# Optimization experiments

Hardware: AMD Instinct MI355X
Metric: run time of the kernel (lower is better)

Reference implementation:

```python
import jax, jax.numpy as jnp
import numpy as np
import math

HID = 128      # hidden_dim == d_inner (expand=1)
NSTATE = 8     # d_state
K = 4          # scan directions
RANK = math.ceil(HID / 16)  # dt_rank = 8
B, H, W = 4, 64, 64


def _ln(x, g, b, eps=1e-5):
    m = jnp.mean(x, -1, keepdims=True)
    v = jnp.mean((x - m) ** 2, -1, keepdims=True)
    return (x - m) * jax.lax.rsqrt(v + eps) * g + b


def _ss2d(x, in_w, conv_w, conv_b, xproj_w, dt_w, dt_b, A_logs, Ds, ln_g, ln_b, out_w):
    # x: [B,H,W,C] -> VMamba SS2D with d_inner=C, 4-direction selective scan
    Bn, Hh, Ww, C = x.shape
    D, L = C, Hh * Ww
    N = A_logs.shape[-1]
    R = dt_w.shape[-1]
    xz = x @ in_w.T                      # [B,H,W,2D]
    xc, z = jnp.split(xz, 2, axis=-1)
    xc = xc.transpose(0, 3, 1, 2)        # [B,D,H,W]
    xc = jax.lax.conv_general_dilated(xc, conv_w, (1, 1), 'SAME', feature_group_count=D)
    xc = jax.nn.silu(xc + conv_b[None, :, None, None])
    x_hw = xc.reshape(Bn, D, L)
    x_wh = xc.transpose(0, 1, 3, 2).reshape(Bn, D, L)
    xs = jnp.stack([x_hw, x_wh, x_hw[..., ::-1], x_wh[..., ::-1]], 1)  # [B,K,D,L]
    x_dbl = jnp.einsum('bkdl,kcd->bkcl', xs, xproj_w)
    dts, Bs, Cs = x_dbl[:, :, :R], x_dbl[:, :, R:R + N], x_dbl[:, :, R + N:]
    dt = jax.nn.softplus(jnp.einsum('bkrl,kdr->bkdl', dts, dt_w) + dt_b[None, :, :, None])
    A = -jnp.exp(A_logs.reshape(K, D, N))  # [K,D,N]

    def step(h, inp):
        x_t, dt_t, B_t, C_t = inp          # [B,K,D],[B,K,D],[B,K,N],[B,K,N]
        h = h * jnp.exp(dt_t[..., None] * A) + dt_t[..., None] * B_t[:, :, None, :] * x_t[..., None]
        return h, jnp.einsum('bkdn,bkn->bkd', h, C_t)

    h0 = jnp.zeros((Bn, K, D, N), x.dtype)
    _, ys = jax.lax.scan(step, h0, (xs.transpose(3, 0, 1, 2), dt.transpose(3, 0, 1, 2),
                                    Bs.transpose(3, 0, 1, 2), Cs.transpose(3, 0, 1, 2)))
    out_y = ys.transpose(1, 2, 3, 0) + Ds.reshape(K, D)[None, :, :, None] * xs  # [B,K,D,L]
    wh_y = out_y[:, 3, :, ::-1].reshape(Bn, D, Ww, Hh).transpose(0, 1, 3, 2).reshape(Bn, D, L)
    invwh_y = out_y[:, 1].reshape(Bn, D, Ww, Hh).transpose(0, 1, 3, 2).reshape(Bn, D, L)
    y = out_y[:, 0] + out_y[:, 2, :, ::-1] + wh_y + invwh_y
    y = _ln(y.transpose(0, 2, 1).reshape(Bn, Hh, Ww, D), ln_g, ln_b)
    return (y * jax.nn.silu(z)) @ out_w.T


def _enhance(x, g, b, w, bias):
    return jax.nn.gelu(_ln(x, g, b) @ w.T + bias, approximate=False)


def setup_inputs() -> dict:
    key = jax.random.key(0)
    ks = jax.random.split(key, 12)
    f = lambda k, s, sc=0.02: jax.random.normal(k, s, jnp.float32) * sc
    return dict(
        sar_feat=jax.random.normal(ks[0], (B, H, W, HID), jnp.float32),
        opt_feat=jax.random.normal(ks[1], (B, H, W, HID), jnp.float32),
        ss_in_w=f(ks[2], (2, 2 * HID, HID)),
        ss_conv_w=f(ks[3], (2, HID, 1, 3, 3), 0.1),
        ss_conv_b=f(ks[4], (2, HID)),
        ss_xproj_w=f(ks[5], (2, K, RANK + 2 * NSTATE, HID)),
        ss_dt_w=f(ks[6], (2, K, HID, RANK), 0.1),
        ss_dt_b=f(ks[7], (2, K, HID), 0.1),
        ss_Alogs=jnp.tile(jnp.log(jnp.arange(1, NSTATE + 1, dtype=jnp.float32)), (2, K * HID, 1)),
        ss_Ds=jnp.ones((2, K * HID), jnp.float32),
        ss_ln_g=jnp.ones((2, HID), jnp.float32),
        ss_ln_b=jnp.zeros((2, HID), jnp.float32),
        ss_out_w=f(ks[8], (2, HID, HID)),
        enh_ln_g=jnp.ones((2, HID), jnp.float32),
        enh_ln_b=jnp.zeros((2, HID), jnp.float32),
        enh_w=f(ks[9], (2, HID, HID)),
        enh_b=jnp.zeros((2, HID), jnp.float32),
    )


def reference(sar_feat, opt_feat, ss_in_w, ss_conv_w, ss_conv_b, ss_xproj_w, ss_dt_w,
              ss_dt_b, ss_Alogs, ss_Ds, ss_ln_g, ss_ln_b, ss_out_w,
              enh_ln_g, enh_ln_b, enh_w, enh_b):
    # cat([opt,sar],-1)[...,:C] == opt ; cat([sar,opt],-1)[...,:C] == sar (faithful identity slice)
    # index 0 = cross_ss2d_s2o (input opt), index 1 = cross_ss2d_o2s (input sar)
    xin = jnp.stack([opt_feat, sar_feat])
    guided = jax.vmap(_ss2d)(xin, ss_in_w, ss_conv_w, ss_conv_b, ss_xproj_w, ss_dt_w,
                             ss_dt_b, ss_Alogs, ss_Ds, ss_ln_g, ss_ln_b, ss_out_w)
    # enhance params: index 0 = enhance_sar (on sar_guided=guided[1]), index 1 = enhance_opt (on opt_guided=guided[0])
    enh_in = jnp.stack([guided[1], guided[0]])
    enhanced = jax.vmap(_enhance)(enh_in, enh_ln_g, enh_ln_b, enh_w, enh_b)
    return (sar_feat + enhanced[0], opt_feat + enhanced[1])
```

## Files before the change

kernel.cpp:

```cpp
#include <hip/hip_runtime.h>
#include <hip/hip_bf16.h>
#include <math.h>

#define DEV __device__ __forceinline__

static constexpr int LL = 4096;
static constexpr int DD = 128;
static constexpr int SEG = 128;
static constexpr float LOG2E = 1.4426950408889634f;
static constexpr float LN2 = 0.6931471805599453f;

DEV float silu_(float x) { return x / (1.f + __expf(-x)); }
DEV float erf_(float x) {
  const float ax = fabsf(x);
  const float t = 1.f / fmaf(0.3275911f, ax, 1.f);
  float p = fmaf(1.061405429f, t, -1.453152027f);
  p = fmaf(p, t, 1.421413741f);
  p = fmaf(p, t, -0.284496736f);
  p = fmaf(p, t, 0.254829592f);
  p = p * t;
  const float r = 1.f - p * __expf(-ax * ax);
  return x < 0.f ? -r : r;
}
DEV float gelu_(float x) { return 0.5f * x * (1.f + erf_(x * 0.7071067811865475f)); }
DEV float sp_(float x) {
  const float t = __builtin_amdgcn_exp2f(-fabsf(x) * LOG2E);
  return fmaxf(x, 0.f) + LN2 * __builtin_amdgcn_logf(1.f + t);
}

template <int CTRL>
DEV float dpp_add_(float x) {
  int y = __builtin_amdgcn_update_dpp(0, __float_as_int(x), CTRL, 0xF, 0xF, true);
  return x + __int_as_float(y);
}

DEV void seg_base_step(int k, int s, int& base, int& step) {
  if (k == 0)      { base = s * 64;        step = 1;   }
  else if (k == 1) { base = s;             step = 64;  }
  else if (k == 2) { base = 4095 - s * 64; step = -1;  }
  else             { base = 4095 - s;      step = -64; }
}

__global__ __launch_bounds__(256) void k_inproj(
    const float* __restrict__ sar, const float* __restrict__ opt,
    const float* __restrict__ in_w, float* __restrict__ xz) {
  const int lt = blockIdx.x, ct = blockIdx.y, mb = blockIdx.z;
  const int m = mb >> 2;
  const float* __restrict__ x = (m == 0 ? opt : sar) + (size_t)(mb & 3) * (LL * DD);
  const float* __restrict__ W = in_w + (size_t)m * 256 * DD;
  __shared__ float sA[64][68];
  __shared__ float sW[64][68];
  const int tid = threadIdx.x;
  const int tc = tid & 15, tl = tid >> 4;
  float acc[4][4] = {};
  for (int db = 0; db < 2; ++db) {
    __syncthreads();
    for (int idx = tid; idx < 64 * 16; idx += 256) {
      const int r = idx >> 4, d4 = (idx & 15) << 2;
      *(float4*)&sA[r][d4] = *(const float4*)&x[(size_t)(lt * 64 + r) * DD + db * 64 + d4];
      *(float4*)&sW[r][d4] = *(const float4*)&W[(size_t)(ct * 64 + r) * DD + db * 64 + d4];
    }
    __syncthreads();
#pragma unroll 4
    for (int d = 0; d < 64; d += 4) {
      float4 a[4], w[4];
#pragma unroll
      for (int q = 0; q < 4; ++q) a[q] = *(const float4*)&sA[tl * 4 + q][d];
#pragma unroll
      for (int j = 0; j < 4; ++j) w[j] = *(const float4*)&sW[tc + 16 * j][d];
#pragma unroll
      for (int j = 0; j < 4; ++j)
#pragma unroll
        for (int q = 0; q < 4; ++q)
          acc[j][q] += a[q].x * w[j].x + a[q].y * w[j].y + a[q].z * w[j].z + a[q].w * w[j].w;
    }
  }
  float* __restrict__ dst = xz + ((size_t)mb * 256 + ct * 64) * LL + lt * 64;
#pragma unroll
  for (int j = 0; j < 4; ++j) {
    float4 v = make_float4(acc[j][0], acc[j][1], acc[j][2], acc[j][3]);
    *(float4*)&dst[(size_t)(tc + 16 * j) * LL + tl * 4] = v;
  }
}

__global__ __launch_bounds__(256) void k_conv(
    const float* __restrict__ xz, const float* __restrict__ conv_w,
    const float* __restrict__ conv_b, float* __restrict__ xc) {
  const int ht = blockIdx.x, dg = blockIdx.y, mb = blockIdx.z;
  const int m = mb >> 2;
  __shared__ float sIn[8][18][66];
  __shared__ float sOut[1024][8];
  const float* __restrict__ src = xz + ((size_t)mb * 256 + dg * 8) * LL;
  const int tid = threadIdx.x;
  for (int idx = tid; idx < 8 * 18 * 66; idx += 256) {
    const int dd = idx / (18 * 66);
    const int rem = idx - dd * (18 * 66);
    const int hh = rem / 66, ww = rem - hh * 66;
    const int h = ht * 16 + hh - 1, w = ww - 1;
    float v = 0.f;
    if (h >= 0 && h < 64 && w >= 0 && w < 64) v = src[(size_t)dd * LL + h * 64 + w];
    sIn[dd][hh][ww] = v;
  }
  __syncthreads();
  const int dd = tid & 7, wv = tid >> 3;
  const int dch = dg * 8 + dd;
  float wk[9];
#pragma unroll
  for (int t = 0; t < 9; ++t) wk[t] = conv_w[((size_t)m * DD + dch) * 9 + t];
  const float bias = conv_b[m * DD + dch];
  for (int hh = 0; hh < 16; ++hh) {
#pragma unroll
    for (int wh = 0; wh < 2; ++wh) {
      const int w = wv + wh * 32;
      float s = bias;
#pragma unroll
      for (int kh = 0; kh < 3; ++kh)
#pragma unroll
        for (int kw = 0; kw < 3; ++kw)
          s = fmaf(sIn[dd][hh + kh][w + kw], wk[kh * 3 + kw], s);
      sOut[hh * 64 + w][dd] = silu_(s);
    }
  }
  __syncthreads();
  float* __restrict__ dst = xc + (size_t)mb * LL * DD + dg * 8;
#pragma unroll
  for (int r = 0; r < 4; ++r) {
    const int pos = tid + r * 256;
    const int l = ht * 1024 + pos;
    *(float4*)&dst[(size_t)l * DD + 0] = *(const float4*)&sOut[pos][0];
    *(float4*)&dst[(size_t)l * DD + 4] = *(const float4*)&sOut[pos][4];
  }
}

__global__ __launch_bounds__(256) void k_xproj(
    const float* __restrict__ xc, const float* __restrict__ xproj_w,
    float* __restrict__ xdbl) {
  const int lt = blockIdx.x, k = blockIdx.y, mb = blockIdx.z;
  const int m = mb >> 2, mbk = mb * 4 + k;
  __shared__ float sX[64][132];
  __shared__ float sW[24][132];
  const int tid = threadIdx.x;
  const float* __restrict__ src = xc + (size_t)mb * LL * DD;
  int base, step;
  seg_base_step(k, lt, base, step);
  for (int idx = tid; idx < 64 * 32; idx += 256) {
    const int l = idx >> 5, d4 = (idx & 31) << 2;
    *(float4*)&sX[l][d4] = *(const float4*)&src[(size_t)(base + l * step) * DD + d4];
  }
  const float* __restrict__ Wsrc = xproj_w + ((size_t)m * 4 + k) * 24 * DD;
  for (int idx = tid; idx < 24 * 32; idx += 256) {
    const int r = idx >> 5, d4 = (idx & 31) << 2;
    *(float4*)&sW[r][d4] = *(const float4*)&Wsrc[(size_t)r * DD + d4];
  }
  __syncthreads();
  const int l = tid >> 2, cg = tid & 3;
  float acc[6] = {};
#pragma unroll 8
  for (int d = 0; d < 128; d += 4) {
    const float4 xv = *(const float4*)&sX[l][d];
#pragma unroll
    for (int j = 0; j < 6; ++j) {
      const float4 wv = *(const float4*)&sW[cg * 6 + j][d];
      acc[j] += xv.x * wv.x + xv.y * wv.y + xv.z * wv.z + xv.w * wv.w;
    }
  }
  float* __restrict__ dst = xdbl + ((size_t)mbk * LL + lt * 64 + l) * 24 + cg * 6;
#pragma unroll
  for (int j = 0; j < 6; ++j) dst[j] = acc[j];
}


DEV void load_aln2(const float* __restrict__ Alogs, int m, int k, int d,
                   float* __restrict__ aln2, bool& fastp) {
  const float4 a0 = *(const float4*)&Alogs[((size_t)m * 512 + k * DD + d) * 8];
  const float4 a1 = *(const float4*)&Alogs[((size_t)m * 512 + k * DD + d) * 8 + 4];
  aln2[0] = -__expf(a0.x) * LOG2E; aln2[1] = -__expf(a0.y) * LOG2E;
  aln2[2] = -__expf(a0.z) * LOG2E; aln2[3] = -__expf(a0.w) * LOG2E;
  aln2[4] = -__expf(a1.x) * LOG2E; aln2[5] = -__expf(a1.y) * LOG2E;
  aln2[6] = -__expf(a1.z) * LOG2E; aln2[7] = -__expf(a1.w) * LOG2E;
  fastp = true;
#pragma unroll
  for (int n = 1; n < 8; ++n)
    fastp = fastp && (fabsf(aln2[n] - (float)(n + 1) * aln2[0]) <=
                      1e-4f * fabsf(aln2[n]) + 1e-12f);
}

DEV void load_w8(const float* __restrict__ dt_w, int mbk, int d,
                 float* __restrict__ wreg) {
  const float4 w0 = *(const float4*)&dt_w[((size_t)mbk * DD + d) * 8];
  const float4 w1 = *(const float4*)&dt_w[((size_t)mbk * DD + d) * 8 + 4];
  wreg[0] = w0.x; wreg[1] = w0.y; wreg[2] = w0.z; wreg[3] = w0.w;
  wreg[4] = w1.x; wreg[5] = w1.y; wreg[6] = w1.z; wreg[7] = w1.w;
}

template <bool FAST>
DEV void qpow_(float dt, const float* __restrict__ aln2, float* __restrict__ q) {
  if constexpr (FAST) {
    q[0] = __builtin_amdgcn_exp2f(dt * aln2[0]);
    q[1] = q[0] * q[0]; q[2] = q[1] * q[0]; q[3] = q[1] * q[1];
    q[4] = q[3] * q[0]; q[5] = q[3] * q[1]; q[6] = q[3] * q[2]; q[7] = q[3] * q[3];
  } else {
#pragma unroll
    for (int n = 0; n < 8; ++n) q[n] = __builtin_amdgcn_exp2f(dt * aln2[n]);
  }
}

DEV float dt_of_(const float* __restrict__ t24,
                 const float* __restrict__ w, float bw) {
  const float4 t0 = *(const float4*)&t24[0];
  const float4 t1 = *(const float4*)&t24[4];
  float s = bw;
  s = fmaf(t0.x, w[0], s); s = fmaf(t0.y, w[1], s);
  s = fmaf(t0.z, w[2], s); s = fmaf(t0.w, w[3], s);
  s = fmaf(t1.x, w[4], s); s = fmaf(t1.y, w[5], s);
  s = fmaf(t1.z, w[6], s); s = fmaf(t1.w, w[7], s);
  return sp_(s);
}

template <bool FAST>
DEV void hstep_(const float* __restrict__ t24, float dt, float x,
                const float* __restrict__ aln2, float* __restrict__ h) {
  const float u = dt * x;
  float q[8];
  qpow_<FAST>(dt, aln2, q);
  const float4 b0 = *(const float4*)&t24[8];
  const float4 b1 = *(const float4*)&t24[12];
  h[0] = fmaf(h[0], q[0], u * b0.x);
  h[1] = fmaf(h[1], q[1], u * b0.y);
  h[2] = fmaf(h[2], q[2], u * b0.z);
  h[3] = fmaf(h[3], q[3], u * b0.w);
  h[4] = fmaf(h[4], q[4], u * b1.x);
  h[5] = fmaf(h[5], q[5], u * b1.y);
  h[6] = fmaf(h[6], q[6], u * b1.z);
  h[7] = fmaf(h[7], q[7], u * b1.w);
}

template <bool FAST>
DEV float ystep_(const float* __restrict__ t24, float dt, float x,
                 const float* __restrict__ aln2, float dsv,
                 float* __restrict__ h) {
  const float u = dt * x;
  float q[8];
  qpow_<FAST>(dt, aln2, q);
  const float4 b0 = *(const float4*)&t24[8];
  const float4 b1 = *(const float4*)&t24[12];
  const float4 c0 = *(const float4*)&t24[16];
  const float4 c1 = *(const float4*)&t24[20];
  float y = dsv * x;
  h[0] = fmaf(h[0], q[0], u * b0.x); y = fmaf(h[0], c0.x, y);
  h[1] = fmaf(h[1], q[1], u * b0.y); y = fmaf(h[1], c0.y, y);
  h[2] = fmaf(h[2], q[2], u * b0.z); y = fmaf(h[2], c0.z, y);
  h[3] = fmaf(h[3], q[3], u * b0.w); y = fmaf(h[3], c0.w, y);
  h[4] = fmaf(h[4], q[4], u * b1.x); y = fmaf(h[4], c1.x, y);
  h[5] = fmaf(h[5], q[5], u * b1.y); y = fmaf(h[5], c1.y, y);
  h[6] = fmaf(h[6], q[6], u * b1.z); y = fmaf(h[6], c1.z, y);
  h[7] = fmaf(h[7], q[7], u * b1.w); y = fmaf(h[7], c1.w, y);
  return y;
}

template <bool FAST>
DEV void loop1d_(const float* __restrict__ tA, const float* __restrict__ tB,
                 const float* __restrict__ sx, int d,
                 const float* __restrict__ aln2A, const float* __restrict__ aln2B,
                 const float* __restrict__ wA, const float* __restrict__ wB,
                 float bwA, float bwB, float* __restrict__ hA,
                 float* __restrict__ hB, float& dtsA, float& dtsB) {
#pragma unroll 8
  for (int j = 0; j < 32; ++j) {
    const float xA = sx[j * 128 + d];
    const float xB = sx[(31 - j) * 128 + d];
    const float dtA = dt_of_(tA + j * 24, wA, bwA);
    const float dtB = dt_of_(tB + j * 24, wB, bwB);
    dtsA += dtA; dtsB += dtB;
    hstep_<FAST>(tA + j * 24, dtA, xA, aln2A, hA);
    hstep_<FAST>(tB + j * 24, dtB, xB, aln2B, hB);
  }
}

__global__ __launch_bounds__(128) void k_scan1(
    const float* __restrict__ xc, const float* __restrict__ xdbl,
    const float* __restrict__ dt_w, const float* __restrict__ dt_b,
    const float* __restrict__ Alogs, float* __restrict__ hend,
    float* __restrict__ Pseg) {
  const int s = blockIdx.x, p = blockIdx.y, mb = blockIdx.z;
  const int m = mb >> 2;
  const int kA = p, kB = p + 2;
  const int sA = s, sB = 127 - s;
  const int mbkA = mb * 4 + kA, mbkB = mb * 4 + kB;
  const int d = threadIdx.x;
  __shared__ float sx[32 * 128];

  const float* __restrict__ tA = xdbl + ((size_t)mbkA * LL + sA * 32) * 24;
  const float* __restrict__ tB = xdbl + ((size_t)mbkB * LL + sB * 32) * 24;

  const int base0 = (p == 0) ? s * 32 : ((s & 1) * 32) * 64 + (s >> 1);
  const int stepPos = (p == 0) ? 1 : 64;
  const float* __restrict__ xsrc = xc + (size_t)mb * LL * DD;
#pragma unroll
  for (int t = 0; t < 8; ++t) {
    const int idx = d + t * 128;
    const int r = idx >> 5, c4 = (idx & 31) << 2;
    ((float4*)sx)[idx] = *(const float4*)&xsrc[(size_t)(base0 + r * stepPos) * DD + c4];
  }

  float aln2A[8], aln2B[8]; bool fA, fB;
  load_aln2(Alogs, m, kA, d, aln2A, fA);
  load_aln2(Alogs, m, kB, d, aln2B, fB);
  float wA[8], wB[8];
  load_w8(dt_w, mbkA, d, wA);
  load_w8(dt_w, mbkB, d, wB);
  const float bwA = dt_b[(size_t)mbkA * DD + d];
  const float bwB = dt_b[(size_t)mbkB * DD + d];
  __syncthreads();

  float hA[8] = {0, 0, 0, 0, 0, 0, 0, 0};
  float hB[8] = {0, 0, 0, 0, 0, 0, 0, 0};
  float dtsA = 0.f, dtsB = 0.f;
  if (fA && fB)
    loop1d_<true>(tA, tB, sx, d, aln2A, aln2B, wA, wB, bwA, bwB, hA, hB, dtsA, dtsB);
  else
    loop1d_<false>(tA, tB, sx, d, aln2A, aln2B, wA, wB, bwA, bwB, hA, hB, dtsA, dtsB);

  {
    float* __restrict__ he = hend + (((size_t)mbkA * SEG + sA) << 10) + d * 8;
    float* __restrict__ pe = Pseg + (((size_t)mbkA * SEG + sA) << 10) + d * 8;
    *(float4*)&he[0] = make_float4(hA[0], hA[1], hA[2], hA[3]);
    *(float4*)&he[4] = make_float4(hA[4], hA[5], hA[6], hA[7]);
    *(float4*)&pe[0] = make_float4(
        __builtin_amdgcn_exp2f(aln2A[0] * dtsA), __builtin_amdgcn_exp2f(aln2A[1] * dtsA),
        __builtin_amdgcn_exp2f(aln2A[2] * dtsA), __builtin_amdgcn_exp2f(aln2A[3] * dtsA));
    *(float4*)&pe[4] = make_float4(
        __builtin_amdgcn_exp2f(aln2A[4] * dtsA), __builtin_amdgcn_exp2f(aln2A[5] * dtsA),
        __builtin_amdgcn_exp2f(aln2A[6] * dtsA), __builtin_amdgcn_exp2f(aln2A[7] * dtsA));
  }
  {
    float* __restrict__ he = hend + (((size_t)mbkB * SEG + sB) << 10) + d * 8;
    float* __restrict__ pe = Pseg + (((size_t)mbkB * SEG + sB) << 10) + d * 8;
    *(float4*)&he[0] = make_float4(hB[0], hB[1], hB[2], hB[3]);
    *(float4*)&he[4] = make_float4(hB[4], hB[5], hB[6], hB[7]);
    *(float4*)&pe[0] = make_float4(
        __builtin_amdgcn_exp2f(aln2B[0] * dtsB), __builtin_amdgcn_exp2f(aln2B[1] * dtsB),
        __builtin_amdgcn_exp2f(aln2B[2] * dtsB), __builtin_amdgcn_exp2f(aln2B[3] * dtsB));
    *(float4*)&pe[4] = make_float4(
        __builtin_amdgcn_exp2f(aln2B[4] * dtsB), __builtin_amdgcn_exp2f(aln2B[5] * dtsB),
        __builtin_amdgcn_exp2f(aln2B[6] * dtsB), __builtin_amdgcn_exp2f(aln2B[7] * dtsB));
  }
}

__global__ __launch_bounds__(256) void k_scan2(
    const float* __restrict__ hend, const float* __restrict__ Pseg,
    float* __restrict__ hin) {
  const int gid = blockIdx.x * 256 + threadIdx.x;
  const int mbk = gid >> 10, dn = gid & 1023;
  const float* __restrict__ P = Pseg + ((size_t)mbk * SEG << 10) + dn;
  const float* __restrict__ E = hend + ((size_t)mbk * SEG << 10) + dn;
  float* __restrict__ O = hin + ((size_t)mbk * SEG << 10) + dn;
  float h = 0.f;
  for (int c0 = 0; c0 < SEG; c0 += 16) {
    float pv[16], ev[16];
#pragma unroll
    for (int t = 0; t < 16; ++t) {
      pv[t] = P[(size_t)(c0 + t) << 10];
      ev[t] = E[(size_t)(c0 + t) << 10];
    }
#pragma unroll
    for (int t = 0; t < 16; ++t) {
      O[(size_t)(c0 + t) << 10] = h;
      h = fmaf(pv[t], h, ev[t]);
    }
  }
}

template <bool FAST>
DEV void chainA_(const float* __restrict__ t24, const float* __restrict__ sx, int d,
                 const float* __restrict__ aln2, const float* __restrict__ w,
                 float bw, float dsv, float* __restrict__ h,
                 float* __restrict__ va) {
#pragma unroll
  for (int j = 0; j < 32; ++j) {
    const float x = sx[j * 128 + d];
    const float dt = dt_of_(t24 + j * 24, w, bw);
    va[j] = ystep_<FAST>(t24 + j * 24, dt, x, aln2, dsv, h);
  }
}

template <bool FAST>
DEV void chainB_(const float* __restrict__ t24, const float* __restrict__ sx, int d,
                 const float* __restrict__ aln2, const float* __restrict__ w,
                 float bw, float dsv, float* __restrict__ h,
                 const float* __restrict__ va, float* __restrict__ yd,
                 ptrdiff_t sstep) {
#pragma unroll
  for (int j = 0; j < 32; ++j) {
    const int phys = 31 - j;
    const float x = sx[phys * 128 + d];
    const float dt = dt_of_(t24 + j * 24, w, bw);
    const float v = ystep_<FAST>(t24 + j * 24, dt, x, aln2, dsv, h);
    yd[(ptrdiff_t)phys * sstep] = v + va[phys];
  }
}

__global__ __launch_bounds__(128) void k_scan3(
    const float* __restrict__ xc, const float* __restrict__ xdbl,
    const float* __restrict__ dt_w, const float* __restrict__ dt_b,
    const float* __restrict__ Alogs, const float* __restrict__ Ds,
    const float* __restrict__ hin, float* __restrict__ yrow,
    float* __restrict__ ycol) {
  const int s = blockIdx.x, p = blockIdx.y, mb = blockIdx.z;
  const int m = mb >> 2;
  const int kA = p, kB = p + 2;
  const int sA = s, sB = 127 - s;
  const int mbkA = mb * 4 + kA, mbkB = mb * 4 + kB;
  const int d = threadIdx.x;
  __shared__ float sx[32 * 128];

  const float* __restrict__ tA = xdbl + ((size_t)mbkA * LL + sA * 32) * 24;
  const float* __restrict__ tB = xdbl + ((size_t)mbkB * LL + sB * 32) * 24;

  const int base0 = (p == 0) ? s * 32 : ((s & 1) * 32) * 64 + (s >> 1);
  const int stepPos = (p == 0) ? 1 : 64;
  const float* __restrict__ xsrc = xc + (size_t)mb * LL * DD;
#pragma unroll
  for (int t = 0; t < 8; ++t) {
    const int idx = d + t * 128;
    const int r = idx >> 5, c4 = (idx & 31) << 2;
    ((float4*)sx)[idx] = *(const float4*)&xsrc[(size_t)(base0 + r * stepPos) * DD + c4];
  }

  float aln2A[8], aln2B[8]; bool fA, fB;
  load_aln2(Alogs, m, kA, d, aln2A, fA);
  load_aln2(Alogs, m, kB, d, aln2B, fB);
  float wA[8], wB[8];
  load_w8(dt_w, mbkA, d, wA);
  load_w8(dt_w, mbkB, d, wB);
  const float bwA = dt_b[(size_t)mbkA * DD + d];
  const float bwB = dt_b[(size_t)mbkB * DD + d];
  const float dsvA = Ds[(size_t)m * 512 + kA * DD + d];
  const float dsvB = Ds[(size_t)m * 512 + kB * DD + d];

  float hA[8], hB[8];
  {
    const float* hp = hin + (((size_t)mbkA * SEG + sA) << 10) + d * 8;
    const float4 h0 = *(const float4*)&hp[0];
    const float4 h1 = *(const float4*)&hp[4];
    hA[0] = h0.x; hA[1] = h0.y; hA[2] = h0.z; hA[3] = h0.w;
    hA[4] = h1.x; hA[5] = h1.y; hA[6] = h1.z; hA[7] = h1.w;
  }
  {
    const float* hp = hin + (((size_t)mbkB * SEG + sB) << 10) + d * 8;
    const float4 h0 = *(const float4*)&hp[0];
    const float4 h1 = *(const float4*)&hp[4];
    hB[0] = h0.x; hB[1] = h0.y; hB[2] = h0.z; hB[3] = h0.w;
    hB[4] = h1.x; hB[5] = h1.y; hB[6] = h1.z; hB[7] = h1.w;
  }

  const size_t off0 = (size_t)mb * LL * DD + (size_t)base0 * DD + d;
  float* __restrict__ yd = (p == 0 ? yrow : ycol) + off0;
  const ptrdiff_t sstep = (ptrdiff_t)stepPos * DD;
  __syncthreads();

  float va[32];
  if (fA) chainA_<true>(tA, sx, d, aln2A, wA, bwA, dsvA, hA, va);
  else    chainA_<false>(tA, sx, d, aln2A, wA, bwA, dsvA, hA, va);
  if (fB) chainB_<true>(tB, sx, d, aln2B, wB, bwB, dsvB, hB, va, yd, sstep);
  else    chainB_<false>(tB, sx, d, aln2B, wB, bwB, dsvB, hB, va, yd, sstep);
}

__global__ __launch_bounds__(256) void k_outproj(
    const float* __restrict__ yrow, const float* __restrict__ ycol,
    const float* __restrict__ xz, const float* __restrict__ ln_g,
    const float* __restrict__ ln_b, const float* __restrict__ out_w,
    float* __restrict__ guided) {
  const int lt = blockIdx.x, mb = blockIdx.y;
  const int m = mb >> 2;
  __shared__ float sv[32][132];
  __shared__ float sW[64][68];
  __shared__ float smr[32][2];
  __shared__ float sg[128], sb[128];
  const int tid = threadIdx.x;
  const size_t yoff = ((size_t)mb * LL + lt * 32) * DD;
  const float4* p0 = (const float4*)(yrow + yoff);
  const float4* p1 = (const float4*)(ycol + yoff);
  float4 ya[4], yb[4];
#pragma unroll
  for (int t = 0; t < 4; ++t) { ya[t] = p0[tid + t * 256]; yb[t] = p1[tid + t * 256]; }
  const int zc = tid >> 1, zh = tid & 1;
  const float4* zsrc = (const float4*)(xz + ((size_t)mb * 256 + 128 + zc) * LL + lt * 32 + zh * 16);
  float4 zv[4];
#pragma unroll
  for (int t = 0; t < 4; ++t) zv[t] = zsrc[t];
  const float* __restrict__ Wp = out_w + (size_t)m * DD * DD;
  float4 wpre[4];
#pragma unroll
  for (int t = 0; t < 4; ++t) {
    const int idx = tid + t * 256;
    wpre[t] = *(const float4*)&Wp[(size_t)(idx >> 4) * DD + ((idx & 15) << 2)];
  }
  if (tid < 128) { sg[tid] = ln_g[m * DD + tid]; sb[tid] = ln_b[m * DD + tid]; }
#pragma unroll
  for (int t = 0; t < 4; ++t) {
    const int idx = tid + t * 256;
    float4 v;
    v.x = ya[t].x + yb[t].x; v.y = ya[t].y + yb[t].y;
    v.z = ya[t].z + yb[t].z; v.w = ya[t].w + yb[t].w;
    *(float4*)&sv[idx >> 5][(idx & 31) << 2] = v;
  }
  __syncthreads();
  {
    const int l = tid >> 3, q = tid & 7;
    float s = 0.f, s2 = 0.f;
#pragma unroll
    for (int d0 = 0; d0 < 16; d0 += 4) {
      const float4 v = *(const float4*)&sv[l][q * 16 + d0];
      s += v.x + v.y + v.z + v.w;
      s2 += v.x * v.x + v.y * v.y + v.z * v.z + v.w * v.w;
    }
    s = dpp_add_<0xB1>(s); s = dpp_add_<0x4E>(s); s = dpp_add_<0x141>(s);
    s2 = dpp_add_<0xB1>(s2); s2 = dpp_add_<0x4E>(s2); s2 = dpp_add_<0x141>(s2);
    if (q == 0) {
      const float mean = s * (1.f / 128.f);
      smr[l][0] = mean;
      smr[l][1] = rsqrtf(fmaf(s2, 1.f / 128.f, -mean * mean) + 1e-5f);
    }
  }
  __syncthreads();
  {
    const float g = sg[zc], bb = sb[zc];
    const float* zf = (const float*)zv;
#pragma unroll
    for (int i2 = 0; i2 < 16; ++i2) {
      const int l = zh * 16 + i2;
      const float v = fmaf((sv[l][zc] - smr[l][0]) * smr[l][1], g, bb);
      sv[l][zc] = v * silu_(zf[i2]);
    }
  }
  const int tc = tid & 15, tl = tid >> 4;
  float* __restrict__ dst = guided + ((size_t)mb * LL + lt * 32) * DD;
#pragma unroll
  for (int jb = 0; jb < 2; ++jb) {
    float acc[4][2] = {};
#pragma unroll
    for (int db = 0; db < 2; ++db) {
      __syncthreads();
#pragma unroll
      for (int t = 0; t < 4; ++t) {
        const int idx = tid + t * 256;
        *(float4*)&sW[idx >> 4][(idx & 15) << 2] = wpre[t];
      }
      const int ph = jb * 2 + db + 1;
      if (ph < 4) {
        const int jb2 = ph >> 1, db2 = ph & 1;
#pragma unroll
        for (int t = 0; t < 4; ++t) {
          const int idx = tid + t * 256;
          wpre[t] = *(const float4*)&Wp[(size_t)(jb2 * 64 + (idx >> 4)) * DD + db2 * 64 + ((idx & 15) << 2)];
        }
      }
      __syncthreads();
#pragma unroll 4
      for (int d0 = 0; d0 < 64; d0 += 4) {
        float4 av[2], wv[4];
#pragma unroll
        for (int q = 0; q < 2; ++q) av[q] = *(const float4*)&sv[tl * 2 + q][db * 64 + d0];
#pragma unroll
        for (int j = 0; j < 4; ++j) wv[j] = *(const float4*)&sW[tc + 16 * j][d0];
#pragma unroll
        for (int j = 0; j < 4; ++j)
#pragma unroll
          for (int q = 0; q < 2; ++q)
            acc[j][q] += av[q].x * wv[j].x + av[q].y * wv[j].y + av[q].z * wv[j].z + av[q].w * wv[j].w;
      }
    }
#pragma unroll
    for (int j = 0; j < 4; ++j)
#pragma unroll
      for (int q = 0; q < 2; ++q)
        dst[(size_t)(tl * 2 + q) * DD + jb * 64 + tc + 16 * j] = acc[j][q];
  }
}

__global__ __launch_bounds__(256) void k_enhance(
    const float* __restrict__ guided, const float* __restrict__ eg,
    const float* __restrict__ ebv, const float* __restrict__ ew,
    const float* __restrict__ ebias, const float* __restrict__ sar,
    const float* __restrict__ opt, float* __restrict__ outp) {
  const int lt = blockIdx.x, ib = blockIdx.y;
  const int i = ib >> 2, b = ib & 3;
  __shared__ float sv[32][132];
  __shared__ float sW[64][68];
  __shared__ float smr[32][2];
  __shared__ float sg[128], sb2[128], sbias[128];
  const int tid = threadIdx.x;
  const float4* gsrc =
      (const float4*)(guided + (((size_t)(1 - i) * 4 + b) * LL + lt * 32) * DD);
  float4 gv[4];
#pragma unroll
  for (int t = 0; t < 4; ++t) gv[t] = gsrc[tid + t * 256];
  const float* __restrict__ Wp = ew + (size_t)i * DD * DD;
  float4 wpre[4];
#pragma unroll
  for (int t = 0; t < 4; ++t) {
    const int idx = tid + t * 256;
    wpre[t] = *(const float4*)&Wp[(size_t)(idx >> 4) * DD + ((idx & 15) << 2)];
  }
  if (tid < 128) {
    sg[tid] = eg[i * DD + tid];
    sb2[tid] = ebv[i * DD + tid];
    sbias[tid] = ebias[i * DD + tid];
  }
#pragma unroll
  for (int t = 0; t < 4; ++t) {
    const int idx = tid + t * 256;
    *(float4*)&sv[idx >> 5][(idx & 31) << 2] = gv[t];
  }
  __syncthreads();
  {
    const int l = tid >> 3, q = tid & 7;
    float s = 0.f, s2 = 0.f;
#pragma unroll
    for (int d0 = 0; d0 < 16; d0 += 4) {
      const float4 v = *(const float4*)&sv[l][q * 16 + d0];
      s += v.x + v.y + v.z + v.w;
      s2 += v.x * v.x + v.y * v.y + v.z * v.z + v.w * v.w;
    }
    s = dpp_add_<0xB1>(s); s = dpp_add_<0x4E>(s); s = dpp_add_<0x141>(s);
    s2 = dpp_add_<0xB1>(s2); s2 = dpp_add_<0x4E>(s2); s2 = dpp_add_<0x141>(s2);
    if (q == 0) {
      const float mean = s * (1.f / 128.f);
      smr[l][0] = mean;
      smr[l][1] = rsqrtf(fmaf(s2, 1.f / 128.f, -mean * mean) + 1e-5f);
    }
  }
  __syncthreads();
  {
    const int c = tid >> 1, half = tid & 1;
    const float g = sg[c], bb = sb2[c];
#pragma unroll
    for (int i2 = 0; i2 < 16; ++i2) {
      const int l = half * 16 + i2;
      sv[l][c] = fmaf((sv[l][c] - smr[l][0]) * smr[l][1], g, bb);
    }
  }
  const int tc = tid & 15, tl = tid >> 4;
  const float* __restrict__ resid = (i == 0 ? sar : opt) + ((size_t)b * LL + lt * 32) * DD;
  float* __restrict__ dst = outp + (size_t)i * (4 * LL * DD) + ((size_t)b * LL + lt * 32) * DD;
  float rv[16];
#pragma unroll
  for (int jb = 0; jb < 2; ++jb)
#pragma unroll
    for (int j = 0; j < 4; ++j)
#pragma unroll
      for (int q = 0; q < 2; ++q)
        rv[jb * 8 + j * 2 + q] = resid[(size_t)(tl * 2 + q) * DD + jb * 64 + tc + 16 * j];
  float accA[4][2] = {}, accB[4][2] = {};
#pragma unroll
  for (int jb = 0; jb < 2; ++jb) {
#pragma unroll
    for (int db = 0; db < 2; ++db) {
      __syncthreads();
#pragma unroll
      for (int t = 0; t < 4; ++t) {
        const int idx = tid + t * 256;
        *(float4*)&sW[idx >> 4][(idx & 15) << 2] = wpre[t];
      }
      const int ph = jb * 2 + db + 1;
      if (ph < 4) {
        const int jb2 = ph >> 1, db2 = ph & 1;
#pragma unroll
        for (int t = 0; t < 4; ++t) {
          const int idx = tid + t * 256;
          wpre[t] = *(const float4*)&Wp[(size_t)(jb2 * 64 + (idx >> 4)) * DD + db2 * 64 + ((idx & 15) << 2)];
        }
      }
      __syncthreads();
      float (*acc)[2] = (jb == 0) ? accA : accB;
#pragma unroll 4
      for (int d0 = 0; d0 < 64; d0 += 4) {
        float4 av[2], wv[4];
#pragma unroll
        for (int q = 0; q < 2; ++q) av[q] = *(const float4*)&sv[tl * 2 + q][db * 64 + d0];
#pragma unroll
        for (int j = 0; j < 4; ++j) wv[j] = *(const float4*)&sW[tc + 16 * j][d0];
#pragma unroll
        for (int j = 0; j < 4; ++j)
#pragma unroll
          for (int q = 0; q < 2; ++q)
            acc[j][q] += av[q].x * wv[j].x + av[q].y * wv[j].y + av[q].z * wv[j].z + av[q].w * wv[j].w;
      }
    }
  }
#pragma unroll
  for (int jb = 0; jb < 2; ++jb)
#pragma unroll
    for (int j = 0; j < 4; ++j)
#pragma unroll
      for (int q = 0; q < 2; ++q) {
        const int col = jb * 64 + tc + 16 * j;
        const float u = ((jb == 0) ? accA[j][q] : accB[j][q]) + sbias[col];
        dst[(size_t)(tl * 2 + q) * DD + col] = rv[jb * 8 + j * 2 + q] + gelu_(u);
      }
}

extern "C" void kernel_launch(void* const* d_in, const int* in_sizes, int n_in,
                              void* d_out, int out_size, void* d_ws, size_t ws_size,
                              hipStream_t stream) {
  (void)in_sizes; (void)n_in; (void)out_size; (void)ws_size;
  const float* sar    = (const float*)d_in[0];
  const float* opt    = (const float*)d_in[1];
  const float* in_w   = (const float*)d_in[2];
  const float* conv_w = (const float*)d_in[3];
  const float* conv_b = (const float*)d_in[4];
  const float* xproj_w= (const float*)d_in[5];
  const float* dt_w   = (const float*)d_in[6];
  const float* dt_b   = (const float*)d_in[7];
  const float* Alogs  = (const float*)d_in[8];
  const float* Ds     = (const float*)d_in[9];
  const float* ln_g   = (const float*)d_in[10];
  const float* ln_b   = (const float*)d_in[11];
  const float* out_w  = (const float*)d_in[12];
  const float* eg     = (const float*)d_in[13];
  const float* eb     = (const float*)d_in[14];
  const float* ew     = (const float*)d_in[15];
  const float* ebias  = (const float*)d_in[16];

  float* ws     = (float*)d_ws;
  float* xz     = ws;
  float* xc     = xz + 8388608;
  float* xdbl   = xc + 4194304;
  float* yrowb  = xdbl + 3145728;
  float* ycolb  = yrowb + 4194304;
  float* guided = ycolb + 4194304;
  float* hend   = guided + 4194304;
  float* Pseg   = hend + 4194304;
  float* hin    = Pseg + 4194304;
  float* outf   = (float*)d_out;

  k_inproj <<<dim3(64, 4, 8), 256, 0, stream>>>(sar, opt, in_w, xz);
  k_conv   <<<dim3(4, 16, 8), 256, 0, stream>>>(xz, conv_w, conv_b, xc);
  k_xproj  <<<dim3(64, 4, 8), 256, 0, stream>>>(xc, xproj_w, xdbl);
  k_scan1  <<<dim3(128, 2, 8), 128, 0, stream>>>(xc, xdbl, dt_w, dt_b, Alogs, hend, Pseg);
  k_scan2  <<<dim3(128), 256, 0, stream>>>(hend, Pseg, hin);
  k_scan3  <<<dim3(128, 2, 8), 128, 0, stream>>>(xc, xdbl, dt_w, dt_b, Alogs, Ds, hin,
                                                 yrowb, ycolb);
  k_outproj<<<dim3(128, 8), 256, 0, stream>>>(yrowb, ycolb, xz, ln_g, ln_b, out_w, guided);
  k_enhance<<<dim3(128, 8), 256, 0, stream>>>(guided, eg, eb, ew, ebias, sar, opt, outf);
}
```

Before: 265.4 us.

## Halve scan segment length, interleave paired-direction chains, and fuse xproj direction pairs

The chunked selective scan moves from 128 segments of 32 steps to 256 segments of 16 steps, doubling the number of scan blocks and shortening each serial chain. Scan3 now runs the forward and reversed direction chains interleaved for more instruction-level parallelism, rather than one after the other. The xproj kernel computes both paired directions from one shared load of xc, and the scan2 prefix result is written in place over hend instead of a separate hin buffer. In exchange, the cross-segment prefix pass in scan2 gets twice as long and more hend/Pseg traffic is needed.

```diff
diff --git a/kernel.cpp b/kernel.cpp
--- a/kernel.cpp
+++ b/kernel.cpp
@@ -6,7 +6,7 @@
 
 static constexpr int LL = 4096;
 static constexpr int DD = 128;
-static constexpr int SEG = 128;
+static constexpr int SEG = 256;
 static constexpr float LOG2E = 1.4426950408889634f;
 static constexpr float LN2 = 0.6931471805599453f;
 
@@ -135,38 +135,46 @@
 __global__ __launch_bounds__(256) void k_xproj(
     const float* __restrict__ xc, const float* __restrict__ xproj_w,
     float* __restrict__ xdbl) {
-  const int lt = blockIdx.x, k = blockIdx.y, mb = blockIdx.z;
-  const int m = mb >> 2, mbk = mb * 4 + k;
+  const int lt = blockIdx.x, p = blockIdx.y, mb = blockIdx.z;
+  const int m = mb >> 2;
+  const int mbkA = mb * 4 + p, mbkB = mb * 4 + p + 2;
   __shared__ float sX[64][132];
-  __shared__ float sW[24][132];
+  __shared__ float sWA[24][132];
+  __shared__ float sWB[24][132];
   const int tid = threadIdx.x;
   const float* __restrict__ src = xc + (size_t)mb * LL * DD;
   int base, step;
-  seg_base_step(k, lt, base, step);
+  seg_base_step(p, lt, base, step);
   for (int idx = tid; idx < 64 * 32; idx += 256) {
     const int l = idx >> 5, d4 = (idx & 31) << 2;
     *(float4*)&sX[l][d4] = *(const float4*)&src[(size_t)(base + l * step) * DD + d4];
   }
-  const float* __restrict__ Wsrc = xproj_w + ((size_t)m * 4 + k) * 24 * DD;
+  const float* __restrict__ WsA = xproj_w + ((size_t)m * 4 + p) * 24 * DD;
+  const float* __restrict__ WsB = xproj_w + ((size_t)m * 4 + p + 2) * 24 * DD;
   for (int idx = tid; idx < 24 * 32; idx += 256) {
     const int r = idx >> 5, d4 = (idx & 31) << 2;
-    *(float4*)&sW[r][d4] = *(const float4*)&Wsrc[(size_t)r * DD + d4];
+    *(float4*)&sWA[r][d4] = *(const float4*)&WsA[(size_t)r * DD + d4];
+    *(float4*)&sWB[r][d4] = *(const float4*)&WsB[(size_t)r * DD + d4];
   }
   __syncthreads();
   const int l = tid >> 2, cg = tid & 3;
-  float acc[6] = {};
+  float acc[6] = {}, acc2[6] = {};
 #pragma unroll 8
   for (int d = 0; d < 128; d += 4) {
     const float4 xv = *(const float4*)&sX[l][d];
 #pragma unroll
     for (int j = 0; j < 6; ++j) {
-      const float4 wv = *(const float4*)&sW[cg * 6 + j][d];
-      acc[j] += xv.x * wv.x + xv.y * wv.y + xv.z * wv.z + xv.w * wv.w;
-    }
-  }
-  float* __restrict__ dst = xdbl + ((size_t)mbk * LL + lt * 64 + l) * 24 + cg * 6;
-#pragma unroll
-  for (int j = 0; j < 6; ++j) dst[j] = acc[j];
+      const float4 wa = *(const float4*)&sWA[cg * 6 + j][d];
+      const float4 wb = *(const float4*)&sWB[cg * 6 + j][d];
+      acc[j] += xv.x * wa.x + xv.y * wa.y + xv.z * wa.z + xv.w * wa.w;
+      acc2[j] += xv.x * wb.x + xv.y * wb.y + xv.z * wb.z + xv.w * wb.w;
+    }
+  }
+  const int rowA = lt * 64 + l;
+  float* __restrict__ dstA = xdbl + ((size_t)mbkA * LL + rowA) * 24 + cg * 6;
+  float* __restrict__ dstB = xdbl + ((size_t)mbkB * LL + (4095 - rowA)) * 24 + cg * 6;
+#pragma unroll
+  for (int j = 0; j < 6; ++j) { dstA[j] = acc[j]; dstB[j] = acc2[j]; }
 }
 
 
@@ -258,6 +266,11 @@
   return y;
 }
 
+DEV void strip16_(int p, int s, int& base, int& stepPos) {
+  if (p == 0) { base = s * 16;                             stepPos = 1;  }
+  else        { base = ((s & 3) * 16) * 64 + (s >> 2);     stepPos = 64; }
+}
+
 template <bool FAST>
 DEV void loop1d_(const float* __restrict__ tA, const float* __restrict__ tB,
                  const float* __restrict__ sx, int d,
@@ -265,10 +278,10 @@
                  const float* __restrict__ wA, const float* __restrict__ wB,
                  float bwA, float bwB, float* __restrict__ hA,
                  float* __restrict__ hB, float& dtsA, float& dtsB) {
-#pragma unroll 8
-  for (int j = 0; j < 32; ++j) {
+#pragma unroll
+  for (int j = 0; j < 16; ++j) {
     const float xA = sx[j * 128 + d];
-    const float xB = sx[(31 - j) * 128 + d];
+    const float xB = sx[(15 - j) * 128 + d];
     const float dtA = dt_of_(tA + j * 24, wA, bwA);
     const float dtB = dt_of_(tB + j * 24, wB, bwB);
     dtsA += dtA; dtsB += dtB;
@@ -285,19 +298,19 @@
   const int s = blockIdx.x, p = blockIdx.y, mb = blockIdx.z;
   const int m = mb >> 2;
   const int kA = p, kB = p + 2;
-  const int sA = s, sB = 127 - s;
+  const int sA = s, sB = 255 - s;
   const int mbkA = mb * 4 + kA, mbkB = mb * 4 + kB;
   const int d = threadIdx.x;
-  __shared__ float sx[32 * 128];
-
-  const float* __restrict__ tA = xdbl + ((size_t)mbkA * LL + sA * 32) * 24;
-  const float* __restrict__ tB = xdbl + ((size_t)mbkB * LL + sB * 32) * 24;
-
-  const int base0 = (p == 0) ? s * 32 : ((s & 1) * 32) * 64 + (s >> 1);
-  const int stepPos = (p == 0) ? 1 : 64;
+  __shared__ float sx[16 * 128];
+
+  const float* __restrict__ tA = xdbl + ((size_t)mbkA * LL + sA * 16) * 24;
+  const float* __restrict__ tB = xdbl + ((size_t)mbkB * LL + sB * 16) * 24;
+
+  int base0, stepPos;
+  strip16_(p, s, base0, stepPos);
   const float* __restrict__ xsrc = xc + (size_t)mb * LL * DD;
 #pragma unroll
-  for (int t = 0; t < 8; ++t) {
+  for (int t = 0; t < 4; ++t) {
     const int idx = d + t * 128;
     const int r = idx >> 5, c4 = (idx & 31) << 2;
     ((float4*)sx)[idx] = *(const float4*)&xsrc[(size_t)(base0 + r * stepPos) * DD + c4];
@@ -348,13 +361,11 @@
 }
 
 __global__ __launch_bounds__(256) void k_scan2(
-    const float* __restrict__ hend, const float* __restrict__ Pseg,
-    float* __restrict__ hin) {
+    float* __restrict__ hend, const float* __restrict__ Pseg) {
   const int gid = blockIdx.x * 256 + threadIdx.x;
   const int mbk = gid >> 10, dn = gid & 1023;
   const float* __restrict__ P = Pseg + ((size_t)mbk * SEG << 10) + dn;
-  const float* __restrict__ E = hend + ((size_t)mbk * SEG << 10) + dn;
-  float* __restrict__ O = hin + ((size_t)mbk * SEG << 10) + dn;
+  float* __restrict__ E = hend + ((size_t)mbk * SEG << 10) + dn;
   float h = 0.f;
   for (int c0 = 0; c0 < SEG; c0 += 16) {
     float pv[16], ev[16];
@@ -365,38 +376,28 @@
     }
 #pragma unroll
     for (int t = 0; t < 16; ++t) {
-      O[(size_t)(c0 + t) << 10] = h;
+      E[(size_t)(c0 + t) << 10] = h;
       h = fmaf(pv[t], h, ev[t]);
     }
   }
 }
 
 template <bool FAST>
-DEV void chainA_(const float* __restrict__ t24, const float* __restrict__ sx, int d,
-                 const float* __restrict__ aln2, const float* __restrict__ w,
-                 float bw, float dsv, float* __restrict__ h,
-                 float* __restrict__ va) {
-#pragma unroll
-  for (int j = 0; j < 32; ++j) {
-    const float x = sx[j * 128 + d];
-    const float dt = dt_of_(t24 + j * 24, w, bw);
-    va[j] = ystep_<FAST>(t24 + j * 24, dt, x, aln2, dsv, h);
-  }
-}
-
-template <bool FAST>
-DEV void chainB_(const float* __restrict__ t24, const float* __restrict__ sx, int d,
-                 const float* __restrict__ aln2, const float* __restrict__ w,
-                 float bw, float dsv, float* __restrict__ h,
-                 const float* __restrict__ va, float* __restrict__ yd,
-                 ptrdiff_t sstep) {
-#pragma unroll
-  for (int j = 0; j < 32; ++j) {
-    const int phys = 31 - j;
-    const float x = sx[phys * 128 + d];
-    const float dt = dt_of_(t24 + j * 24, w, bw);
-    const float v = ystep_<FAST>(t24 + j * 24, dt, x, aln2, dsv, h);
-    yd[(ptrdiff_t)phys * sstep] = v + va[phys];
+DEV void loop3i_(const float* __restrict__ tA, const float* __restrict__ tB,
+                 const float* __restrict__ sx, int d,
+                 const float* __restrict__ aln2A, const float* __restrict__ aln2B,
+                 const float* __restrict__ wA, const float* __restrict__ wB,
+                 float bwA, float bwB, float dsvA, float dsvB,
+                 float* __restrict__ hA, float* __restrict__ hB,
+                 float* __restrict__ va, float* __restrict__ vb) {
+#pragma unroll
+  for (int j = 0; j < 16; ++j) {
+    const float xA = sx[j * 128 + d];
+    const float xB = sx[(15 - j) * 128 + d];
+    const float dtA = dt_of_(tA + j * 24, wA, bwA);
+    const float dtB = dt_of_(tB + j * 24, wB, bwB);
+    va[j] = ystep_<FAST>(tA + j * 24, dtA, xA, aln2A, dsvA, hA);
+    vb[j] = ystep_<FAST>(tB + j * 24, dtB, xB, aln2B, dsvB, hB);
   }
 }
 
@@ -409,19 +410,19 @@
   const int s = blockIdx.x, p = blockIdx.y, mb = blockIdx.z;
   const int m = mb >> 2;
   const int kA = p, kB = p + 2;
-  const int sA = s, sB = 127 - s;
+  const int sA = s, sB = 255 - s;
   const int mbkA = mb * 4 + kA, mbkB = mb * 4 + kB;
   const int d = threadIdx.x;
-  __shared__ float sx[32 * 128];
-
-  const float* __restrict__ tA = xdbl + ((size_t)mbkA * LL + sA * 32) * 24;
-  const float* __restrict__ tB = xdbl + ((size_t)mbkB * LL + sB * 32) * 24;
-
-  const int base0 = (p == 0) ? s * 32 : ((s & 1) * 32) * 64 + (s >> 1);
-  const int stepPos = (p == 0) ? 1 : 64;
+  __shared__ float sx[16 * 128];
+
+  const float* __restrict__ tA = xdbl + ((size_t)mbkA * LL + sA * 16) * 24;
+  const float* __restrict__ tB = xdbl + ((size_t)mbkB * LL + sB * 16) * 24;
+
+  int base0, stepPos;
+  strip16_(p, s, base0, stepPos);
   const float* __restrict__ xsrc = xc + (size_t)mb * LL * DD;
 #pragma unroll
-  for (int t = 0; t < 8; ++t) {
+  for (int t = 0; t < 4; ++t) {
     const int idx = d + t * 128;
     const int r = idx >> 5, c4 = (idx & 31) << 2;
     ((float4*)sx)[idx] = *(const float4*)&xsrc[(size_t)(base0 + r * stepPos) * DD + c4];
@@ -459,11 +460,16 @@
   const ptrdiff_t sstep = (ptrdiff_t)stepPos * DD;
   __syncthreads();
 
-  float va[32];
-  if (fA) chainA_<true>(tA, sx, d, aln2A, wA, bwA, dsvA, hA, va);
-  else    chainA_<false>(tA, sx, d, aln2A, wA, bwA, dsvA, hA, va);
-  if (fB) chainB_<true>(tB, sx, d, aln2B, wB, bwB, dsvB, hB, va, yd, sstep);
-  else    chainB_<false>(tB, sx, d, aln2B, wB, bwB, dsvB, hB, va, yd, sstep);
+  float va[16], vb[16];
+  if (fA && fB)
+    loop3i_<true>(tA, tB, sx, d, aln2A, aln2B, wA, wB, bwA, bwB,
+                  dsvA, dsvB, hA, hB, va, vb);
+  else
+    loop3i_<false>(tA, tB, sx, d, aln2A, aln2B, wA, wB, bwA, bwB,
+                   dsvA, dsvB, hA, hB, va, vb);
+#pragma unroll
+  for (int phys = 0; phys < 16; ++phys)
+    yd[(ptrdiff_t)phys * sstep] = va[phys] + vb[15 - phys];
 }
 
 __global__ __launch_bounds__(256) void k_outproj(
@@ -731,16 +737,15 @@
   float* ycolb  = yrowb + 4194304;
   float* guided = ycolb + 4194304;
   float* hend   = guided + 4194304;
-  float* Pseg   = hend + 4194304;
-  float* hin    = Pseg + 4194304;
+  float* Pseg   = hend + 8388608;
   float* outf   = (float*)d_out;
 
   k_inproj <<<dim3(64, 4, 8), 256, 0, stream>>>(sar, opt, in_w, xz);
   k_conv   <<<dim3(4, 16, 8), 256, 0, stream>>>(xz, conv_w, conv_b, xc);
-  k_xproj  <<<dim3(64, 4, 8), 256, 0, stream>>>(xc, xproj_w, xdbl);
-  k_scan1  <<<dim3(128, 2, 8), 128, 0, stream>>>(xc, xdbl, dt_w, dt_b, Alogs, hend, Pseg);
-  k_scan2  <<<dim3(128), 256, 0, stream>>>(hend, Pseg, hin);
-  k_scan3  <<<dim3(128, 2, 8), 128, 0, stream>>>(xc, xdbl, dt_w, dt_b, Alogs, Ds, hin,
+  k_xproj  <<<dim3(64, 2, 8), 256, 0, stream>>>(xc, xproj_w, xdbl);
+  k_scan1  <<<dim3(256, 2, 8), 128, 0, stream>>>(xc, xdbl, dt_w, dt_b, Alogs, hend, Pseg);
+  k_scan2  <<<dim3(128), 256, 0, stream>>>(hend, Pseg);
+  k_scan3  <<<dim3(256, 2, 8), 128, 0, stream>>>(xc, xdbl, dt_w, dt_b, Alogs, Ds, hend,
                                                  yrowb, ycolb);
   k_outproj<<<dim3(128, 8), 256, 0, stream>>>(yrowb, ycolb, xz, ln_g, ln_b, out_w, guided);
   k_enhance<<<dim3(128, 8), 256, 0, stream>>>(guided, eg, eb, ew, ebias, sar, opt, outf);
```

New measurement: 303.5 us. +14.4%, slower.
